# Kernel optimization log

Measured on AMD Instinct MI355X. Metric: run time of the kernel, lower is better.

Reference implementation:

```python
import jax, jax.numpy as jnp
import numpy as np

NUM_EXPERTS = 64
TOP_K = 8
HIDDEN = 2048
MLP = 768
TOKENS = 1024


def setup_inputs() -> dict:
    key = jax.random.key(0)
    ks = jax.random.split(key, 5)
    hidden_states = jax.random.normal(ks[0], (TOKENS, HIDDEN), dtype=jnp.float32)
    # lecun-normal-ish scaling (std = 1/sqrt(fan_in))
    router_w = jax.random.normal(ks[1], (HIDDEN, NUM_EXPERTS), dtype=jnp.float32) / np.sqrt(HIDDEN)
    gate_proj = jax.random.normal(ks[2], (NUM_EXPERTS, HIDDEN, MLP), dtype=jnp.float32) / np.sqrt(HIDDEN)
    up_proj = jax.random.normal(ks[3], (NUM_EXPERTS, HIDDEN, MLP), dtype=jnp.float32) / np.sqrt(HIDDEN)
    down_proj = jax.random.normal(ks[4], (NUM_EXPERTS, MLP, HIDDEN), dtype=jnp.float32) / np.sqrt(MLP)
    return {
        "hidden_states": hidden_states,
        "router_w": router_w,
        "gate_proj": gate_proj,
        "up_proj": up_proj,
        "down_proj": down_proj,
    }


def reference(hidden_states, router_w, gate_proj, up_proj, down_proj):
    # Router: [T, E]
    router_logits = hidden_states @ router_w
    # Top-k routing, softmax renormalized over the selected k (norm_topk_prob=True)
    routing_weights, selected_experts = jax.lax.top_k(router_logits, k=TOP_K)
    routing_weights = jax.nn.softmax(routing_weights, axis=-1)  # [T, k]

    sel_flat = selected_experts.ravel()  # [T*k] int32
    # Duplicate each token for each of its k experts: [T*k, H]
    x_exp = jnp.repeat(hidden_states, TOP_K, axis=0)

    # prepare_routing: sort token copies by expert id, count per-expert group sizes
    sort_idx = jnp.argsort(sel_flat)          # stable sort of expert ids
    x_sorted = x_exp[sort_idx]                # [T*k, H] grouped by expert
    group_sizes = jnp.zeros((NUM_EXPERTS,), dtype=jnp.int32).at[sel_flat].add(1)
    unsort_idx = jnp.argsort(sort_idx)

    # Grouped GEMMs (megablox-style) via ragged_dot
    gate_out = jax.lax.ragged_dot(x_sorted, gate_proj, group_sizes)   # [T*k, M]
    up_out = jax.lax.ragged_dot(x_sorted, up_proj, group_sizes)       # [T*k, M]
    down_out = jax.lax.ragged_dot(jax.nn.silu(gate_out) * up_out, down_proj, group_sizes)  # [T*k, H]

    # Unsort back to (token, k) order and combine with routing weights
    unsorted = down_out[unsort_idx].reshape(-1, TOP_K, HIDDEN)
    return jnp.sum(unsorted * routing_weights[..., None], axis=1)  # [T, H]
```

## Files before the change

### kernel.cpp

```cpp
#include <hip/hip_runtime.h>
#include <hip/hip_bf16.h>

#define T_TOKENS 1024
#define HID      2048
#define NEXP     64
#define TOPK     8
#define MLP      768
#define NPAIR    (T_TOKENS * TOPK)

typedef __bf16 bf16x8 __attribute__((ext_vector_type(8)));
typedef float  f32x4  __attribute__((ext_vector_type(4)));
typedef unsigned int u32x2 __attribute__((ext_vector_type(2)));
typedef unsigned int u32x4 __attribute__((ext_vector_type(4)));

#define LDK 40

static __device__ __forceinline__ unsigned short f2bf(float f) {
    __hip_bfloat16 h = __float2bfloat16(f);
    unsigned short u;
    __builtin_memcpy(&u, &h, sizeof(u));
    return u;
}
static __device__ __forceinline__ unsigned int pk2bf(float a, float b) {
    return (unsigned int)f2bf(a) | ((unsigned int)f2bf(b) << 16);
}

__global__ __launch_bounds__(256) void router_topk_kernel(
    const float* __restrict__ hs, const float* __restrict__ rw,
    int* __restrict__ sel, float* __restrict__ wts)
{
    const int lane = threadIdx.x & 63;
    const int tg   = threadIdx.x >> 6;
    const int t    = blockIdx.x * 4 + tg;

    const float4* x4 = (const float4*)(hs + (size_t)t * HID);
    float acc = 0.f;
    for (int h4 = 0; h4 < HID / 4; ++h4) {
        float4 xv = x4[h4];
        int hb = h4 * 4 * NEXP + lane;
        acc += xv.x * rw[hb] + xv.y * rw[hb + NEXP]
             + xv.z * rw[hb + 2 * NEXP] + xv.w * rw[hb + 3 * NEXP];
    }

    float v = acc;
    float tv[TOPK]; int ti[TOPK];
    for (int i = 0; i < TOPK; ++i) {
        float m = v; int mi = lane;
        for (int off = 32; off > 0; off >>= 1) {
            float om  = __shfl_xor(m, off, 64);
            int   omi = __shfl_xor(mi, off, 64);
            if (om > m || (om == m && omi < mi)) { m = om; mi = omi; }
        }
        tv[i] = m; ti[i] = mi;
        if (lane == mi) v = -__builtin_inff();
    }
    if (lane == 0) {
        float mx = tv[0], s = 0.f, e[TOPK];
        for (int i = 0; i < TOPK; ++i) { e[i] = __expf(tv[i] - mx); s += e[i]; }
        float inv = 1.f / s;
        for (int i = 0; i < TOPK; ++i) {
            wts[t * TOPK + i] = e[i] * inv;
            sel[t * TOPK + i] = ti[i];
        }
    }
}

__global__ void count_kernel(const int* __restrict__ sel, int* __restrict__ counts)
{
    int p = blockIdx.x * 256 + threadIdx.x;
    if (p < NPAIR) atomicAdd(&counts[sel[p]], 1);
}

__global__ void scan_kernel(const int* __restrict__ counts,
                            int* __restrict__ offsets, int* __restrict__ cursor)
{
    if (threadIdx.x == 0) {
        int s = 0;
        for (int e = 0; e < NEXP; ++e) { offsets[e] = s; cursor[e] = s; s += counts[e]; }
        offsets[NEXP] = s;
    }
}

__global__ void scatter_kernel(const int* __restrict__ sel,
                               int* __restrict__ cursor, int* __restrict__ rows)
{
    int p = blockIdx.x * 256 + threadIdx.x;
    if (p < NPAIR) {
        int e = sel[p];
        int pos = atomicAdd(&cursor[e], 1);
        rows[pos] = p;
    }
}

__global__ __launch_bounds__(512) void gateup_kernel(
    const float* __restrict__ hs, const float* __restrict__ gw,
    const float* __restrict__ uw, const int* __restrict__ offsets,
    const int* __restrict__ rows, unsigned short* __restrict__ hb)
{
    const int e  = blockIdx.y;
    const int n0 = blockIdx.x * 64;
    const int r0 = offsets[e];
    const int nrows = offsets[e + 1] - r0;
    if (nrows <= 0) return;

    __shared__ __align__(16) float smemf[12800];
    unsigned short* smem = (unsigned short*)smemf;

    const int thr  = threadIdx.x;
    const int wave = thr >> 6;
    const int lane = thr & 63;
    const int wg   = wave & 3;
    const int isUp = wave >> 2;
    const int fr   = lane & 15;
    const int fq   = lane >> 4;

    const int ar = thr >> 3;
    const int ac = (thr & 7) * 4;

    const int wk2 = thr & 15;
    const int wnq = (thr & 255) >> 4;
    const float* wsrc = (thr >= 256 ? uw : gw)
        + (size_t)e * HID * MLP + (size_t)(2 * wk2) * MLP + n0 + wnq * 4;
    const int mofs = (thr >= 256) ? 10240 : 7680;

    const int NS = HID / 32;

    for (int m0 = 0; m0 < nrows; m0 += 192) {
        const float *ap0, *ap1, *ap2;
        bool av0, av1, av2;
        {
            int gr0 = m0 + ar, gr1 = m0 + ar + 64, gr2 = m0 + ar + 128;
            av0 = gr0 < nrows; av1 = gr1 < nrows; av2 = gr2 < nrows;
            int p0 = av0 ? rows[r0 + gr0] : 0;
            int p1 = av1 ? rows[r0 + gr1] : 0;
            int p2 = av2 ? rows[r0 + gr2] : 0;
            ap0 = hs + (size_t)(p0 >> 3) * HID + ac;
            ap1 = hs + (size_t)(p1 >> 3) * HID + ac;
            ap2 = hs + (size_t)(p2 >> 3) * HID + ac;
        }

        f32x4 va0, va1, va2, w0, w1;
        const f32x4 fz = (f32x4){0.f, 0.f, 0.f, 0.f};

        auto LOAD = [&](int s) {
            va0 = av0 ? *(const f32x4*)(ap0 + s * 32) : fz;
            va1 = av1 ? *(const f32x4*)(ap1 + s * 32) : fz;
            va2 = av2 ? *(const f32x4*)(ap2 + s * 32) : fz;
            const float* wp = wsrc + (size_t)s * 32 * MLP;
            w0 = *(const f32x4*)wp;
            w1 = *(const f32x4*)(wp + MLP);
        };
        auto WRITE = [&](int s) {
            unsigned short* b = smem + (s & 1) * 12800;
            u32x2 v;
            v[0] = pk2bf(va0[0], va0[1]); v[1] = pk2bf(va0[2], va0[3]);
            *(u32x2*)(b + ar * LDK + ac) = v;
            v[0] = pk2bf(va1[0], va1[1]); v[1] = pk2bf(va1[2], va1[3]);
            *(u32x2*)(b + (ar + 64) * LDK + ac) = v;
            v[0] = pk2bf(va2[0], va2[1]); v[1] = pk2bf(va2[2], va2[3]);
            *(u32x2*)(b + (ar + 128) * LDK + ac) = v;
            unsigned short* wb = b + mofs;
            #pragma unroll
            for (int i = 0; i < 4; ++i)
                *(unsigned int*)(wb + (wnq * 4 + i) * LDK + 2 * wk2) = pk2bf(w0[i], w1[i]);
        };

        f32x4 acc[3][4];
        #pragma unroll
        for (int ms = 0; ms < 3; ++ms)
            #pragma unroll
            for (int ns = 0; ns < 4; ++ns) acc[ms][ns] = fz;

        LOAD(0);
        WRITE(0);
        LOAD(1);
        asm volatile("s_waitcnt lgkmcnt(0)" ::: "memory");
        __builtin_amdgcn_s_barrier();

        for (int s = 0; s < NS; ++s) {
            const unsigned short* bb  = smem + (s & 1) * 12800;
            const unsigned short* wbb = bb + mofs;
            bf16x8 aF0, aF1, aF2, wF[4];
            #pragma unroll
            for (int ns = 0; ns < 4; ++ns)
                wF[ns] = *(const bf16x8*)(wbb + (ns * 16 + fr) * LDK + fq * 8);
            aF0 = *(const bf16x8*)(bb + (wg * 48 + fr) * LDK + fq * 8);
            aF1 = *(const bf16x8*)(bb + (wg * 48 + 16 + fr) * LDK + fq * 8);
            aF2 = *(const bf16x8*)(bb + (wg * 48 + 32 + fr) * LDK + fq * 8);

            if (s + 1 < NS) WRITE(s + 1);
            if (s + 2 < NS) LOAD(s + 2);

            const int rem = nrows - m0 - wg * 48;
            if (rem > 0) {
                #pragma unroll
                for (int ns = 0; ns < 4; ++ns)
                    acc[0][ns] = __builtin_amdgcn_mfma_f32_16x16x32_bf16(aF0, wF[ns], acc[0][ns], 0, 0, 0);
            }
            if (rem > 16) {
                #pragma unroll
                for (int ns = 0; ns < 4; ++ns)
                    acc[1][ns] = __builtin_amdgcn_mfma_f32_16x16x32_bf16(aF1, wF[ns], acc[1][ns], 0, 0, 0);
            }
            if (rem > 32) {
                #pragma unroll
                for (int ns = 0; ns < 4; ++ns)
                    acc[2][ns] = __builtin_amdgcn_mfma_f32_16x16x32_bf16(aF2, wF[ns], acc[2][ns], 0, 0, 0);
            }
            asm volatile("s_waitcnt lgkmcnt(0)" ::: "memory");
            __builtin_amdgcn_s_barrier();
        }

        float* xb = smemf;
        if (isUp) {
            #pragma unroll
            for (int ms = 0; ms < 3; ++ms)
                #pragma unroll
                for (int i = 0; i < 4; ++i) {
                    int lrow = wg * 48 + ms * 16 + fq * 4 + i;
                    #pragma unroll
                    for (int ns = 0; ns < 4; ++ns)
                        xb[lrow * 65 + ns * 16 + fr] = acc[ms][ns][i];
                }
        }
        __syncthreads();
        if (!isUp) {
            #pragma unroll
            for (int ms = 0; ms < 3; ++ms)
                #pragma unroll
                for (int i = 0; i < 4; ++i) {
                    int lrow = wg * 48 + ms * 16 + fq * 4 + i;
                    int grow = m0 + lrow;
                    if (grow < nrows) {
                        unsigned short* drow = hb + (size_t)(r0 + grow) * MLP + n0;
                        #pragma unroll
                        for (int ns = 0; ns < 4; ++ns) {
                            float g = acc[ms][ns][i];
                            float u = xb[lrow * 65 + ns * 16 + fr];
                            float h = g * u / (1.f + __expf(-g));
                            drow[ns * 16 + fr] = f2bf(h);
                        }
                    }
                }
        }
        __syncthreads();
    }
}

__global__ __launch_bounds__(256) void down_kernel(
    const unsigned short* __restrict__ hb, const float* __restrict__ dw,
    const int* __restrict__ offsets, const int* __restrict__ rows,
    const float* __restrict__ wts, float* __restrict__ out)
{
    const int e  = blockIdx.y;
    const int n0 = blockIdx.x * 64;
    const int r0 = offsets[e];
    const int nrows = offsets[e + 1] - r0;
    if (nrows <= 0) return;

    __shared__ __align__(16) float smemf[10240];
    unsigned short* smem = (unsigned short*)smemf;

    const int thr  = threadIdx.x;
    const int wave = thr >> 6;
    const int lane = thr & 63;
    const int fr   = lane & 15;
    const int fq   = lane >> 4;

    const int ar = thr >> 2;
    const int ac = (thr & 3) * 8;

    const int wk2 = thr & 15;
    const int wnq = thr >> 4;
    const float* wsrc = dw + (size_t)e * MLP * HID + (size_t)(2 * wk2) * HID + n0 + wnq * 4;

    const int NS = MLP / 32;

    for (int m0 = 0; m0 < nrows; m0 += 192) {
        const bool av0 = (m0 + ar)       < nrows;
        const bool av1 = (m0 + ar + 64)  < nrows;
        const bool av2 = (m0 + ar + 128) < nrows;
        const unsigned short* hp0 = hb + (size_t)(r0 + m0 + ar) * MLP + ac;
        const unsigned short* hp1 = hp0 + (size_t)64  * MLP;
        const unsigned short* hp2 = hp0 + (size_t)128 * MLP;

        u32x4 ua0, ua1, ua2; f32x4 w0, w1;
        const u32x4 uz = (u32x4){0u, 0u, 0u, 0u};
        const f32x4 fz = (f32x4){0.f, 0.f, 0.f, 0.f};

        auto LOAD = [&](int s) {
            ua0 = av0 ? *(const u32x4*)(hp0 + s * 32) : uz;
            ua1 = av1 ? *(const u32x4*)(hp1 + s * 32) : uz;
            ua2 = av2 ? *(const u32x4*)(hp2 + s * 32) : uz;
            const float* wp = wsrc + (size_t)s * 32 * HID;
            w0 = *(const f32x4*)wp;
            w1 = *(const f32x4*)(wp + HID);
        };
        auto WRITE = [&](int s) {
            unsigned short* b = smem + (s & 1) * 10240;
            *(u32x4*)(b + ar * LDK + ac) = ua0;
            *(u32x4*)(b + (ar + 64) * LDK + ac) = ua1;
            *(u32x4*)(b + (ar + 128) * LDK + ac) = ua2;
            unsigned short* wb = b + 7680;
            #pragma unroll
            for (int i = 0; i < 4; ++i)
                *(unsigned int*)(wb + (wnq * 4 + i) * LDK + 2 * wk2) = pk2bf(w0[i], w1[i]);
        };

        f32x4 acc[3][4];
        #pragma unroll
        for (int ms = 0; ms < 3; ++ms)
            #pragma unroll
            for (int ns = 0; ns < 4; ++ns) acc[ms][ns] = fz;

        LOAD(0);
        WRITE(0);
        LOAD(1);
        asm volatile("s_waitcnt lgkmcnt(0)" ::: "memory");
        __builtin_amdgcn_s_barrier();

        for (int s = 0; s < NS; ++s) {
            const unsigned short* bb = smem + (s & 1) * 10240;
            bf16x8 aF0, aF1, aF2, bF[4];
            #pragma unroll
            for (int ns = 0; ns < 4; ++ns)
                bF[ns] = *(const bf16x8*)(bb + 7680 + (ns * 16 + fr) * LDK + fq * 8);
            aF0 = *(const bf16x8*)(bb + (wave * 48 + fr) * LDK + fq * 8);
            aF1 = *(const bf16x8*)(bb + (wave * 48 + 16 + fr) * LDK + fq * 8);
            aF2 = *(const bf16x8*)(bb + (wave * 48 + 32 + fr) * LDK + fq * 8);

            if (s + 1 < NS) WRITE(s + 1);
            if (s + 2 < NS) LOAD(s + 2);

            const int rem = nrows - m0 - wave * 48;
            if (rem > 0) {
                #pragma unroll
                for (int ns = 0; ns < 4; ++ns)
                    acc[0][ns] = __builtin_amdgcn_mfma_f32_16x16x32_bf16(aF0, bF[ns], acc[0][ns], 0, 0, 0);
            }
            if (rem > 16) {
                #pragma unroll
                for (int ns = 0; ns < 4; ++ns)
                    acc[1][ns] = __builtin_amdgcn_mfma_f32_16x16x32_bf16(aF1, bF[ns], acc[1][ns], 0, 0, 0);
            }
            if (rem > 32) {
                #pragma unroll
                for (int ns = 0; ns < 4; ++ns)
                    acc[2][ns] = __builtin_amdgcn_mfma_f32_16x16x32_bf16(aF2, bF[ns], acc[2][ns], 0, 0, 0);
            }
            asm volatile("s_waitcnt lgkmcnt(0)" ::: "memory");
            __builtin_amdgcn_s_barrier();
        }

        #pragma unroll
        for (int ms = 0; ms < 3; ++ms) {
            #pragma unroll
            for (int i = 0; i < 4; ++i) {
                int lrow = wave * 48 + ms * 16 + fq * 4 + i;
                int grow = m0 + lrow;
                if (grow < nrows) {
                    int p  = rows[r0 + grow];
                    float w = wts[p];
                    float* orow = out + (size_t)(p >> 3) * HID + n0;
                    #pragma unroll
                    for (int ns = 0; ns < 4; ++ns)
                        atomicAdd(orow + ns * 16 + fr, acc[ms][ns][i] * w);
                }
            }
        }
    }
}

extern "C" void kernel_launch(void* const* d_in, const int* in_sizes, int n_in,
                              void* d_out, int out_size, void* d_ws, size_t ws_size,
                              hipStream_t stream)
{
    const float* hs = (const float*)d_in[0];
    const float* rw = (const float*)d_in[1];
    const float* gw = (const float*)d_in[2];
    const float* uw = (const float*)d_in[3];
    const float* dw = (const float*)d_in[4];
    float* out = (float*)d_out;

    char* ws = (char*)d_ws;
    int*   sel     = (int*)(ws);
    float* wts     = (float*)(ws + 32768);
    int*   counts  = (int*)(ws + 65536);
    int*   offsets = (int*)(ws + 65792);
    int*   cursor  = (int*)(ws + 66304);
    int*   rows    = (int*)(ws + 66560);
    unsigned short* hb = (unsigned short*)(ws + 99328);

    hipMemsetAsync(out, 0, (size_t)T_TOKENS * HID * sizeof(float), stream);
    hipMemsetAsync(counts, 0, NEXP * sizeof(int), stream);

    router_topk_kernel<<<T_TOKENS / 4, 256, 0, stream>>>(hs, rw, sel, wts);
    count_kernel<<<NPAIR / 256, 256, 0, stream>>>(sel, counts);
    scan_kernel<<<1, 64, 0, stream>>>(counts, offsets, cursor);
    scatter_kernel<<<NPAIR / 256, 256, 0, stream>>>(sel, cursor, rows);
    gateup_kernel<<<dim3(MLP / 64, NEXP), 512, 0, stream>>>(hs, gw, uw, offsets, rows, hb);
    down_kernel<<<dim3(HID / 64, NEXP), 256, 0, stream>>>(hb, dw, offsets, rows, wts, out);
}
```

Baseline: 1.227 ms.

## Pre-convert activations to bf16, swizzle block order, deepen weight-load pipeline

Adds a kernel that converts hidden_states to bf16 once, so gate/up reads half the activation bytes and skips per-tile conversion. Both grouped GEMM kernels now use a 1D grid with a swizzle that spreads the blocks of one expert across XCD-interleaved positions. The main loop is unrolled by two with separate even/odd weight registers, so global weight loads are issued two stages ahead of use. The price is an extra launch, extra workspace and higher register pressure.

```diff
diff --git a/kernel.cpp b/kernel.cpp
--- a/kernel.cpp
+++ b/kernel.cpp
@@ -23,6 +23,18 @@
 }
 static __device__ __forceinline__ unsigned int pk2bf(float a, float b) {
     return (unsigned int)f2bf(a) | ((unsigned int)f2bf(b) << 16);
+}
+
+__global__ __launch_bounds__(256) void cvt_hs_kernel(
+    const float* __restrict__ hs, unsigned short* __restrict__ xb)
+{
+    int i = (blockIdx.x * 256 + threadIdx.x) * 8;
+    f32x4 a = *(const f32x4*)(hs + i);
+    f32x4 b = *(const f32x4*)(hs + i + 4);
+    u32x4 v;
+    v[0] = pk2bf(a[0], a[1]); v[1] = pk2bf(a[2], a[3]);
+    v[2] = pk2bf(b[0], b[1]); v[3] = pk2bf(b[2], b[3]);
+    *(u32x4*)(xb + i) = v;
 }
 
 __global__ __launch_bounds__(256) void router_topk_kernel(
@@ -93,12 +105,15 @@
 }
 
 __global__ __launch_bounds__(512) void gateup_kernel(
-    const float* __restrict__ hs, const float* __restrict__ gw,
+    const unsigned short* __restrict__ xb, const float* __restrict__ gw,
     const float* __restrict__ uw, const int* __restrict__ offsets,
     const int* __restrict__ rows, unsigned short* __restrict__ hb)
 {
-    const int e  = blockIdx.y;
-    const int n0 = blockIdx.x * 64;
+    const int bid = blockIdx.x;
+    const int sw  = (bid & 7) * 96 + (bid >> 3);
+    const int e   = sw / 12;
+    const int n0  = (sw % 12) * 64;
+
     const int r0 = offsets[e];
     const int nrows = offsets[e + 1] - r0;
     if (nrows <= 0) return;
@@ -126,7 +141,7 @@
     const int NS = HID / 32;
 
     for (int m0 = 0; m0 < nrows; m0 += 192) {
-        const float *ap0, *ap1, *ap2;
+        const unsigned short *ap0, *ap1, *ap2;
         bool av0, av1, av2;
         {
             int gr0 = m0 + ar, gr1 = m0 + ar + 64, gr2 = m0 + ar + 128;
@@ -134,35 +149,46 @@
             int p0 = av0 ? rows[r0 + gr0] : 0;
             int p1 = av1 ? rows[r0 + gr1] : 0;
             int p2 = av2 ? rows[r0 + gr2] : 0;
-            ap0 = hs + (size_t)(p0 >> 3) * HID + ac;
-            ap1 = hs + (size_t)(p1 >> 3) * HID + ac;
-            ap2 = hs + (size_t)(p2 >> 3) * HID + ac;
-        }
-
-        f32x4 va0, va1, va2, w0, w1;
+            ap0 = xb + (size_t)(p0 >> 3) * HID + ac;
+            ap1 = xb + (size_t)(p1 >> 3) * HID + ac;
+            ap2 = xb + (size_t)(p2 >> 3) * HID + ac;
+        }
+
+        u32x2 va0, va1, va2;
+        f32x4 w0e, w1e, w0o, w1o;
+        const u32x2 z2 = (u32x2){0u, 0u};
         const f32x4 fz = (f32x4){0.f, 0.f, 0.f, 0.f};
 
-        auto LOAD = [&](int s) {
-            va0 = av0 ? *(const f32x4*)(ap0 + s * 32) : fz;
-            va1 = av1 ? *(const f32x4*)(ap1 + s * 32) : fz;
-            va2 = av2 ? *(const f32x4*)(ap2 + s * 32) : fz;
+        auto LOAD_A = [&](int s) {
+            va0 = av0 ? *(const u32x2*)(ap0 + s * 32) : z2;
+            va1 = av1 ? *(const u32x2*)(ap1 + s * 32) : z2;
+            va2 = av2 ? *(const u32x2*)(ap2 + s * 32) : z2;
+        };
+        auto WRITE_A = [&](int s) {
+            unsigned short* b = smem + (s & 1) * 12800;
+            *(u32x2*)(b + ar * LDK + ac) = va0;
+            *(u32x2*)(b + (ar + 64) * LDK + ac) = va1;
+            *(u32x2*)(b + (ar + 128) * LDK + ac) = va2;
+        };
+        auto LOAD_WE = [&](int s) {
             const float* wp = wsrc + (size_t)s * 32 * MLP;
-            w0 = *(const f32x4*)wp;
-            w1 = *(const f32x4*)(wp + MLP);
-        };
-        auto WRITE = [&](int s) {
-            unsigned short* b = smem + (s & 1) * 12800;
-            u32x2 v;
-            v[0] = pk2bf(va0[0], va0[1]); v[1] = pk2bf(va0[2], va0[3]);
-            *(u32x2*)(b + ar * LDK + ac) = v;
-            v[0] = pk2bf(va1[0], va1[1]); v[1] = pk2bf(va1[2], va1[3]);
-            *(u32x2*)(b + (ar + 64) * LDK + ac) = v;
-            v[0] = pk2bf(va2[0], va2[1]); v[1] = pk2bf(va2[2], va2[3]);
-            *(u32x2*)(b + (ar + 128) * LDK + ac) = v;
-            unsigned short* wb = b + mofs;
+            w0e = *(const f32x4*)wp;  w1e = *(const f32x4*)(wp + MLP);
+        };
+        auto LOAD_WO = [&](int s) {
+            const float* wp = wsrc + (size_t)s * 32 * MLP;
+            w0o = *(const f32x4*)wp;  w1o = *(const f32x4*)(wp + MLP);
+        };
+        auto WRITE_WE = [&](int s) {
+            unsigned short* wb = smem + (s & 1) * 12800 + mofs;
             #pragma unroll
             for (int i = 0; i < 4; ++i)
-                *(unsigned int*)(wb + (wnq * 4 + i) * LDK + 2 * wk2) = pk2bf(w0[i], w1[i]);
+                *(unsigned int*)(wb + (wnq * 4 + i) * LDK + 2 * wk2) = pk2bf(w0e[i], w1e[i]);
+        };
+        auto WRITE_WO = [&](int s) {
+            unsigned short* wb = smem + (s & 1) * 12800 + mofs;
+            #pragma unroll
+            for (int i = 0; i < 4; ++i)
+                *(unsigned int*)(wb + (wnq * 4 + i) * LDK + 2 * wk2) = pk2bf(w0o[i], w1o[i]);
         };
 
         f32x4 acc[3][4];
@@ -171,14 +197,9 @@
             #pragma unroll
             for (int ns = 0; ns < 4; ++ns) acc[ms][ns] = fz;
 
-        LOAD(0);
-        WRITE(0);
-        LOAD(1);
-        asm volatile("s_waitcnt lgkmcnt(0)" ::: "memory");
-        __builtin_amdgcn_s_barrier();
-
-        for (int s = 0; s < NS; ++s) {
-            const unsigned short* bb  = smem + (s & 1) * 12800;
+        const int rem = nrows - m0 - wg * 48;
+
+        auto DOSTEP = [&](const unsigned short* bb) {
             const unsigned short* wbb = bb + mofs;
             bf16x8 aF0, aF1, aF2, wF[4];
             #pragma unroll
@@ -187,31 +208,75 @@
             aF0 = *(const bf16x8*)(bb + (wg * 48 + fr) * LDK + fq * 8);
             aF1 = *(const bf16x8*)(bb + (wg * 48 + 16 + fr) * LDK + fq * 8);
             aF2 = *(const bf16x8*)(bb + (wg * 48 + 32 + fr) * LDK + fq * 8);
-
-            if (s + 1 < NS) WRITE(s + 1);
-            if (s + 2 < NS) LOAD(s + 2);
-
-            const int rem = nrows - m0 - wg * 48;
-            if (rem > 0) {
-                #pragma unroll
-                for (int ns = 0; ns < 4; ++ns)
-                    acc[0][ns] = __builtin_amdgcn_mfma_f32_16x16x32_bf16(aF0, wF[ns], acc[0][ns], 0, 0, 0);
+            return (void)0, (void)aF0, (void)aF1, (void)aF2, (void)wF;
+        };
+        (void)DOSTEP;
+
+        LOAD_WE(0);
+        LOAD_WO(1);
+        LOAD_A(0);
+        WRITE_WE(0);
+        WRITE_A(0);
+        LOAD_A(1);
+        asm volatile("s_waitcnt lgkmcnt(0)" ::: "memory");
+        __builtin_amdgcn_s_barrier();
+
+        #define GU_MFMA(BB)                                                          \
+        {                                                                            \
+            const unsigned short* wbb = (BB) + mofs;                                 \
+            bf16x8 aF0, aF1, aF2, wF0, wF1, wF2, wF3;                                \
+            wF0 = *(const bf16x8*)(wbb + (0 * 16 + fr) * LDK + fq * 8);              \
+            wF1 = *(const bf16x8*)(wbb + (1 * 16 + fr) * LDK + fq * 8);              \
+            wF2 = *(const bf16x8*)(wbb + (2 * 16 + fr) * LDK + fq * 8);              \
+            wF3 = *(const bf16x8*)(wbb + (3 * 16 + fr) * LDK + fq * 8);              \
+            aF0 = *(const bf16x8*)((BB) + (wg * 48 + fr) * LDK + fq * 8);            \
+            aF1 = *(const bf16x8*)((BB) + (wg * 48 + 16 + fr) * LDK + fq * 8);       \
+            aF2 = *(const bf16x8*)((BB) + (wg * 48 + 32 + fr) * LDK + fq * 8);       \
+            MFMA_BLOCK(aF0, aF1, aF2, wF0, wF1, wF2, wF3)                            \
+        }
+        #define MFMA_BLOCK(A0, A1, A2, W0, W1, W2, W3)                               \
+            if (rem > 0) {                                                           \
+                acc[0][0] = __builtin_amdgcn_mfma_f32_16x16x32_bf16(A0, W0, acc[0][0], 0, 0, 0); \
+                acc[0][1] = __builtin_amdgcn_mfma_f32_16x16x32_bf16(A0, W1, acc[0][1], 0, 0, 0); \
+                acc[0][2] = __builtin_amdgcn_mfma_f32_16x16x32_bf16(A0, W2, acc[0][2], 0, 0, 0); \
+                acc[0][3] = __builtin_amdgcn_mfma_f32_16x16x32_bf16(A0, W3, acc[0][3], 0, 0, 0); \
+            }                                                                        \
+            if (rem > 16) {                                                          \
+                acc[1][0] = __builtin_amdgcn_mfma_f32_16x16x32_bf16(A1, W0, acc[1][0], 0, 0, 0); \
+                acc[1][1] = __builtin_amdgcn_mfma_f32_16x16x32_bf16(A1, W1, acc[1][1], 0, 0, 0); \
+                acc[1][2] = __builtin_amdgcn_mfma_f32_16x16x32_bf16(A1, W2, acc[1][2], 0, 0, 0); \
+                acc[1][3] = __builtin_amdgcn_mfma_f32_16x16x32_bf16(A1, W3, acc[1][3], 0, 0, 0); \
+            }                                                                        \
+            if (rem > 32) {                                                          \
+                acc[2][0] = __builtin_amdgcn_mfma_f32_16x16x32_bf16(A2, W0, acc[2][0], 0, 0, 0); \
+                acc[2][1] = __builtin_amdgcn_mfma_f32_16x16x32_bf16(A2, W1, acc[2][1], 0, 0, 0); \
+                acc[2][2] = __builtin_amdgcn_mfma_f32_16x16x32_bf16(A2, W2, acc[2][2], 0, 0, 0); \
+                acc[2][3] = __builtin_amdgcn_mfma_f32_16x16x32_bf16(A2, W3, acc[2][3], 0, 0, 0); \
             }
-            if (rem > 16) {
-                #pragma unroll
-                for (int ns = 0; ns < 4; ++ns)
-                    acc[1][ns] = __builtin_amdgcn_mfma_f32_16x16x32_bf16(aF1, wF[ns], acc[1][ns], 0, 0, 0);
+
+        for (int s = 0; s < NS; s += 2) {
+            {
+                if (s + 2 < NS) LOAD_WE(s + 2);
+                GU_MFMA(smem)
+                WRITE_WO(s + 1);
+                WRITE_A(s + 1);
+                if (s + 2 < NS) LOAD_A(s + 2);
+                asm volatile("s_waitcnt lgkmcnt(0)" ::: "memory");
+                __builtin_amdgcn_s_barrier();
             }
-            if (rem > 32) {
-                #pragma unroll
-                for (int ns = 0; ns < 4; ++ns)
-                    acc[2][ns] = __builtin_amdgcn_mfma_f32_16x16x32_bf16(aF2, wF[ns], acc[2][ns], 0, 0, 0);
+            {
+                if (s + 3 < NS) LOAD_WO(s + 3);
+                GU_MFMA(smem + 12800)
+                if (s + 2 < NS) { WRITE_WE(s + 2); WRITE_A(s + 2); }
+                if (s + 3 < NS) LOAD_A(s + 3);
+                asm volatile("s_waitcnt lgkmcnt(0)" ::: "memory");
+                __builtin_amdgcn_s_barrier();
             }
-            asm volatile("s_waitcnt lgkmcnt(0)" ::: "memory");
-            __builtin_amdgcn_s_barrier();
-        }
-
-        float* xb = smemf;
+        }
+        #undef GU_MFMA
+        #undef MFMA_BLOCK
+
+        float* xbf = smemf;
         if (isUp) {
             #pragma unroll
             for (int ms = 0; ms < 3; ++ms)
@@ -220,7 +285,7 @@
                     int lrow = wg * 48 + ms * 16 + fq * 4 + i;
                     #pragma unroll
                     for (int ns = 0; ns < 4; ++ns)
-                        xb[lrow * 65 + ns * 16 + fr] = acc[ms][ns][i];
+                        xbf[lrow * 65 + ns * 16 + fr] = acc[ms][ns][i];
                 }
         }
         __syncthreads();
@@ -236,7 +301,7 @@
                         #pragma unroll
                         for (int ns = 0; ns < 4; ++ns) {
                             float g = acc[ms][ns][i];
-                            float u = xb[lrow * 65 + ns * 16 + fr];
+                            float u = xbf[lrow * 65 + ns * 16 + fr];
                             float h = g * u / (1.f + __expf(-g));
                             drow[ns * 16 + fr] = f2bf(h);
                         }
@@ -252,8 +317,11 @@
     const int* __restrict__ offsets, const int* __restrict__ rows,
     const float* __restrict__ wts, float* __restrict__ out)
 {
-    const int e  = blockIdx.y;
-    const int n0 = blockIdx.x * 64;
+    const int bid = blockIdx.x;
+    const int sw  = (bid & 7) * 256 + (bid >> 3);
+    const int e   = sw >> 5;
+    const int n0  = (sw & 31) * 64;
+
     const int r0 = offsets[e];
     const int nrows = offsets[e + 1] - r0;
     if (nrows <= 0) return;
@@ -284,27 +352,41 @@
         const unsigned short* hp1 = hp0 + (size_t)64  * MLP;
         const unsigned short* hp2 = hp0 + (size_t)128 * MLP;
 
-        u32x4 ua0, ua1, ua2; f32x4 w0, w1;
+        u32x4 ua0, ua1, ua2;
+        f32x4 w0e, w1e, w0o, w1o;
         const u32x4 uz = (u32x4){0u, 0u, 0u, 0u};
         const f32x4 fz = (f32x4){0.f, 0.f, 0.f, 0.f};
 
-        auto LOAD = [&](int s) {
+        auto LOAD_A = [&](int s) {
             ua0 = av0 ? *(const u32x4*)(hp0 + s * 32) : uz;
             ua1 = av1 ? *(const u32x4*)(hp1 + s * 32) : uz;
             ua2 = av2 ? *(const u32x4*)(hp2 + s * 32) : uz;
-            const float* wp = wsrc + (size_t)s * 32 * HID;
-            w0 = *(const f32x4*)wp;
-            w1 = *(const f32x4*)(wp + HID);
-        };
-        auto WRITE = [&](int s) {
+        };
+        auto WRITE_A = [&](int s) {
             unsigned short* b = smem + (s & 1) * 10240;
             *(u32x4*)(b + ar * LDK + ac) = ua0;
             *(u32x4*)(b + (ar + 64) * LDK + ac) = ua1;
             *(u32x4*)(b + (ar + 128) * LDK + ac) = ua2;
-            unsigned short* wb = b + 7680;
+        };
+        auto LOAD_WE = [&](int s) {
+            const float* wp = wsrc + (size_t)s * 32 * HID;
+            w0e = *(const f32x4*)wp;  w1e = *(const f32x4*)(wp + HID);
+        };
+        auto LOAD_WO = [&](int s) {
+            const float* wp = wsrc + (size_t)s * 32 * HID;
+            w0o = *(const f32x4*)wp;  w1o = *(const f32x4*)(wp + HID);
+        };
+        auto WRITE_WE = [&](int s) {
+            unsigned short* wb = smem + (s & 1) * 10240 + 7680;
             #pragma unroll
             for (int i = 0; i < 4; ++i)
-                *(unsigned int*)(wb + (wnq * 4 + i) * LDK + 2 * wk2) = pk2bf(w0[i], w1[i]);
+                *(unsigned int*)(wb + (wnq * 4 + i) * LDK + 2 * wk2) = pk2bf(w0e[i], w1e[i]);
+        };
+        auto WRITE_WO = [&](int s) {
+            unsigned short* wb = smem + (s & 1) * 10240 + 7680;
+            #pragma unroll
+            for (int i = 0; i < 4; ++i)
+                *(unsigned int*)(wb + (wnq * 4 + i) * LDK + 2 * wk2) = pk2bf(w0o[i], w1o[i]);
         };
 
         f32x4 acc[3][4];
@@ -313,44 +395,68 @@
             #pragma unroll
             for (int ns = 0; ns < 4; ++ns) acc[ms][ns] = fz;
 
-        LOAD(0);
-        WRITE(0);
-        LOAD(1);
+        const int rem = nrows - m0 - wave * 48;
+
+        LOAD_WE(0);
+        LOAD_WO(1);
+        LOAD_A(0);
+        WRITE_WE(0);
+        WRITE_A(0);
+        LOAD_A(1);
         asm volatile("s_waitcnt lgkmcnt(0)" ::: "memory");
         __builtin_amdgcn_s_barrier();
 
-        for (int s = 0; s < NS; ++s) {
-            const unsigned short* bb = smem + (s & 1) * 10240;
-            bf16x8 aF0, aF1, aF2, bF[4];
-            #pragma unroll
-            for (int ns = 0; ns < 4; ++ns)
-                bF[ns] = *(const bf16x8*)(bb + 7680 + (ns * 16 + fr) * LDK + fq * 8);
-            aF0 = *(const bf16x8*)(bb + (wave * 48 + fr) * LDK + fq * 8);
-            aF1 = *(const bf16x8*)(bb + (wave * 48 + 16 + fr) * LDK + fq * 8);
-            aF2 = *(const bf16x8*)(bb + (wave * 48 + 32 + fr) * LDK + fq * 8);
-
-            if (s + 1 < NS) WRITE(s + 1);
-            if (s + 2 < NS) LOAD(s + 2);
-
-            const int rem = nrows - m0 - wave * 48;
-            if (rem > 0) {
-                #pragma unroll
-                for (int ns = 0; ns < 4; ++ns)
-                    acc[0][ns] = __builtin_amdgcn_mfma_f32_16x16x32_bf16(aF0, bF[ns], acc[0][ns], 0, 0, 0);
+        #define DN_MFMA(BB)                                                          \
+        {                                                                            \
+            const unsigned short* wbb = (BB) + 7680;                                 \
+            bf16x8 aF0, aF1, aF2, wF0, wF1, wF2, wF3;                                \
+            wF0 = *(const bf16x8*)(wbb + (0 * 16 + fr) * LDK + fq * 8);              \
+            wF1 = *(const bf16x8*)(wbb + (1 * 16 + fr) * LDK + fq * 8);              \
+            wF2 = *(const bf16x8*)(wbb + (2 * 16 + fr) * LDK + fq * 8);              \
+            wF3 = *(const bf16x8*)(wbb + (3 * 16 + fr) * LDK + fq * 8);              \
+            aF0 = *(const bf16x8*)((BB) + (wave * 48 + fr) * LDK + fq * 8);          \
+            aF1 = *(const bf16x8*)((BB) + (wave * 48 + 16 + fr) * LDK + fq * 8);     \
+            aF2 = *(const bf16x8*)((BB) + (wave * 48 + 32 + fr) * LDK + fq * 8);     \
+            if (rem > 0) {                                                           \
+                acc[0][0] = __builtin_amdgcn_mfma_f32_16x16x32_bf16(aF0, wF0, acc[0][0], 0, 0, 0); \
+                acc[0][1] = __builtin_amdgcn_mfma_f32_16x16x32_bf16(aF0, wF1, acc[0][1], 0, 0, 0); \
+                acc[0][2] = __builtin_amdgcn_mfma_f32_16x16x32_bf16(aF0, wF2, acc[0][2], 0, 0, 0); \
+                acc[0][3] = __builtin_amdgcn_mfma_f32_16x16x32_bf16(aF0, wF3, acc[0][3], 0, 0, 0); \
+            }                                                                        \
+            if (rem > 16) {                                                          \
+                acc[1][0] = __builtin_amdgcn_mfma_f32_16x16x32_bf16(aF1, wF0, acc[1][0], 0, 0, 0); \
+                acc[1][1] = __builtin_amdgcn_mfma_f32_16x16x32_bf16(aF1, wF1, acc[1][1], 0, 0, 0); \
+                acc[1][2] = __builtin_amdgcn_mfma_f32_16x16x32_bf16(aF1, wF2, acc[1][2], 0, 0, 0); \
+                acc[1][3] = __builtin_amdgcn_mfma_f32_16x16x32_bf16(aF1, wF3, acc[1][3], 0, 0, 0); \
+            }                                                                        \
+            if (rem > 32) {                                                          \
+                acc[2][0] = __builtin_amdgcn_mfma_f32_16x16x32_bf16(aF2, wF0, acc[2][0], 0, 0, 0); \
+                acc[2][1] = __builtin_amdgcn_mfma_f32_16x16x32_bf16(aF2, wF1, acc[2][1], 0, 0, 0); \
+                acc[2][2] = __builtin_amdgcn_mfma_f32_16x16x32_bf16(aF2, wF2, acc[2][2], 0, 0, 0); \
+                acc[2][3] = __builtin_amdgcn_mfma_f32_16x16x32_bf16(aF2, wF3, acc[2][3], 0, 0, 0); \
+            }                                                                        \
+        }
+
+        for (int s = 0; s < NS; s += 2) {
+            {
+                if (s + 2 < NS) LOAD_WE(s + 2);
+                DN_MFMA(smem)
+                WRITE_WO(s + 1);
+                WRITE_A(s + 1);
+                if (s + 2 < NS) LOAD_A(s + 2);
+                asm volatile("s_waitcnt lgkmcnt(0)" ::: "memory");
+                __builtin_amdgcn_s_barrier();
             }
-            if (rem > 16) {
-                #pragma unroll
-                for (int ns = 0; ns < 4; ++ns)
-                    acc[1][ns] = __builtin_amdgcn_mfma_f32_16x16x32_bf16(aF1, bF[ns], acc[1][ns], 0, 0, 0);
+            {
+                if (s + 3 < NS) LOAD_WO(s + 3);
+                DN_MFMA(smem + 10240)
+                if (s + 2 < NS) { WRITE_WE(s + 2); WRITE_A(s + 2); }
+                if (s + 3 < NS) LOAD_A(s + 3);
+                asm volatile("s_waitcnt lgkmcnt(0)" ::: "memory");
+                __builtin_amdgcn_s_barrier();
             }
-            if (rem > 32) {
-                #pragma unroll
-                for (int ns = 0; ns < 4; ++ns)
-                    acc[2][ns] = __builtin_amdgcn_mfma_f32_16x16x32_bf16(aF2, bF[ns], acc[2][ns], 0, 0, 0);
-            }
-            asm volatile("s_waitcnt lgkmcnt(0)" ::: "memory");
-            __builtin_amdgcn_s_barrier();
-        }
+        }
+        #undef DN_MFMA
 
         #pragma unroll
         for (int ms = 0; ms < 3; ++ms) {
@@ -389,15 +495,17 @@
     int*   offsets = (int*)(ws + 65792);
     int*   cursor  = (int*)(ws + 66304);
     int*   rows    = (int*)(ws + 66560);
-    unsigned short* hb = (unsigned short*)(ws + 99328);
+    unsigned short* xb = (unsigned short*)(ws + 99328);
+    unsigned short* hb = (unsigned short*)(ws + 99328 + 4194304);
 
     hipMemsetAsync(out, 0, (size_t)T_TOKENS * HID * sizeof(float), stream);
     hipMemsetAsync(counts, 0, NEXP * sizeof(int), stream);
 
+    cvt_hs_kernel<<<T_TOKENS * HID / (256 * 8), 256, 0, stream>>>(hs, xb);
     router_topk_kernel<<<T_TOKENS / 4, 256, 0, stream>>>(hs, rw, sel, wts);
     count_kernel<<<NPAIR / 256, 256, 0, stream>>>(sel, counts);
     scan_kernel<<<1, 64, 0, stream>>>(counts, offsets, cursor);
     scatter_kernel<<<NPAIR / 256, 256, 0, stream>>>(sel, cursor, rows);
-    gateup_kernel<<<dim3(MLP / 64, NEXP), 512, 0, stream>>>(hs, gw, uw, offsets, rows, hb);
-    down_kernel<<<dim3(HID / 64, NEXP), 256, 0, stream>>>(hb, dw, offsets, rows, wts, out);
-}
+    gateup_kernel<<<768, 512, 0, stream>>>(xb, gw, uw, offsets, rows, hb);
+    down_kernel<<<2048, 256, 0, stream>>>(hb, dw, offsets, rows, wts, out);
+}
```

After: 1.237 ms. Within noise of the previous version (+0.8%).
